# Kernel tuning notes

Hardware: AMD Instinct MI355X
Metric: run time of the kernel (lower is better)

The kernel has to match this reference:

```python
import jax, jax.numpy as jnp
import numpy as np

C = 512
HSIZE = C // 4
D, H, W = 18, 24, 24
N = D * H * W


def setup_inputs() -> dict:
    key = jax.random.key(0)
    ks = jax.random.split(key, 6)
    features = jax.random.normal(ks[0], (1, C, D, H, W), dtype=jnp.float32)
    Wi = jax.random.normal(ks[1], (HSIZE, C), dtype=jnp.float32) * 0.02
    bi = jax.random.normal(ks[2], (HSIZE,), dtype=jnp.float32) * 0.02
    Wj = jax.random.normal(ks[3], (HSIZE, C), dtype=jnp.float32) * 0.02
    bj = jax.random.normal(ks[4], (HSIZE,), dtype=jnp.float32) * 0.02
    # attention_agregate: shape (head=1, 1), xavier-uniform in the original
    agg = jax.random.uniform(ks[5], (1, 1), dtype=jnp.float32, minval=-1.0, maxval=1.0)
    return {"features": features, "Wi": Wi, "bi": bi, "Wj": Wj, "bj": bj, "agg": agg}


def reference(features, Wi, bi, Wj, bj, agg):
    # features: [1, C, D, H, W]; 1x1x1 convs == channel-wise matmuls
    x = features.reshape(C, N)                      # [C, N]
    fi = (Wi @ x + bi[:, None]).T                   # [N, hsize]  (conv_i output, permuted)
    fj = Wj @ x + bj[:, None]                       # [hsize, N]  (conv_j output)
    fk = x.T                                        # [N, C]      (raw features, NOT conv_k)
    # original: attn = (fi @ fj) * agg / N ; out = attn @ fk
    # linear chain reassociated: fi @ (fj @ fk) * agg / N  (same math, no NxN intermediate)
    scale = agg[0, 0] / jnp.float32(N)
    out_flat = (fi @ (fj @ fk)) * scale             # [N, C]
    return features + out_flat.T.reshape(1, C, D, H, W)
```

## Files before the change

### kernel.cpp

```cpp
#include <hip/hip_runtime.h>
#include <hip/hip_bf16.h>

#define C_   512
#define HS   128
#define NN   10368

typedef __bf16 bf16x8 __attribute__((ext_vector_type(8)));
typedef float  f32x4  __attribute__((ext_vector_type(4)));

__global__ void k_transpose(const float* __restrict__ x, __bf16* __restrict__ xbT,
                            float* __restrict__ Mtf) {
    const int b = blockIdx.x;
    const int t = threadIdx.x;
    if (b < 1296) {
        __shared__ float tile[64][65];
        const int c0 = (b & 7) * 64, n0 = (b >> 3) * 64;
        const int tr = t >> 6, tn = t & 63;
        #pragma unroll
        for (int i = 0; i < 16; i++) {
            int c = tr + i * 4;
            tile[c][tn] = x[(size_t)(c0 + c) * NN + n0 + tn];
        }
        __syncthreads();
        #pragma unroll
        for (int i = 0; i < 16; i++) {
            int n = tr + i * 4;
            xbT[(size_t)(n0 + n) * C_ + c0 + tn] = (__bf16)tile[tn][n];
        }
    } else {
        const int j = b - 1296;
        f32x4 z = {0.f, 0.f, 0.f, 0.f};
        float* p = Mtf + j * 4096 + t * 16;
        *(f32x4*)(p)      = z;
        *(f32x4*)(p + 4)  = z;
        *(f32x4*)(p + 8)  = z;
        *(f32x4*)(p + 12) = z;
    }
}

__device__ __forceinline__ bf16x8 load_f32x8_as_bf16(const float* __restrict__ p) {
    float4 v0 = *(const float4*)p;
    float4 v1 = *(const float4*)(p + 4);
    bf16x8 o;
    o[0] = (__bf16)v0.x; o[1] = (__bf16)v0.y; o[2] = (__bf16)v0.z; o[3] = (__bf16)v0.w;
    o[4] = (__bf16)v1.x; o[5] = (__bf16)v1.y; o[6] = (__bf16)v1.z; o[7] = (__bf16)v1.w;
    return o;
}

__global__ void k_gemm12(const __bf16* __restrict__ xbT,
                         const float* __restrict__ Wi, const float* __restrict__ Wj,
                         const float* __restrict__ bi, const float* __restrict__ bj,
                         __bf16* __restrict__ fj, __bf16* __restrict__ finm) {
    const int w    = blockIdx.x * 4 + (threadIdx.x >> 6);
    const int lane = threadIdx.x & 63;
    const int l16  = lane & 15;
    const int q    = lane >> 4;
    if (w < 648) {
        const int h0 = (w & 3) * 32, n0 = (w >> 2) * 64;
        f32x4 acc[2][4] = {};
        for (int k = 0; k < 512; k += 32) {
            bf16x8 a[2], b[4];
            #pragma unroll
            for (int i = 0; i < 2; i++)
                a[i] = load_f32x8_as_bf16(Wj + (h0 + 16 * i + l16) * 512 + k + q * 8);
            #pragma unroll
            for (int tt = 0; tt < 4; tt++)
                b[tt] = *(const bf16x8*)(xbT + (size_t)(n0 + 16 * tt + l16) * 512 + k + q * 8);
            #pragma unroll
            for (int i = 0; i < 2; i++)
                #pragma unroll
                for (int tt = 0; tt < 4; tt++)
                    acc[i][tt] = __builtin_amdgcn_mfma_f32_16x16x32_bf16(a[i], b[tt], acc[i][tt], 0, 0, 0);
        }
        #pragma unroll
        for (int i = 0; i < 2; i++)
            #pragma unroll
            for (int tt = 0; tt < 4; tt++)
                #pragma unroll
                for (int r = 0; r < 4; r++) {
                    int h = h0 + 16 * i + q * 4 + r;
                    int n = n0 + 16 * tt + l16;
                    fj[(size_t)h * NN + n] = (__bf16)(acc[i][tt][r] + bj[h]);
                }
    } else {
        const int w2 = w - 648;
        const int n0 = (w2 >> 2) * 64, h0 = (w2 & 3) * 32;
        f32x4 acc[4][2] = {};
        for (int k = 0; k < 512; k += 32) {
            bf16x8 a[4], b[2];
            #pragma unroll
            for (int i = 0; i < 4; i++)
                a[i] = *(const bf16x8*)(xbT + (size_t)(n0 + 16 * i + l16) * 512 + k + q * 8);
            #pragma unroll
            for (int tt = 0; tt < 2; tt++)
                b[tt] = load_f32x8_as_bf16(Wi + (h0 + 16 * tt + l16) * 512 + k + q * 8);
            #pragma unroll
            for (int i = 0; i < 4; i++)
                #pragma unroll
                for (int tt = 0; tt < 2; tt++)
                    acc[i][tt] = __builtin_amdgcn_mfma_f32_16x16x32_bf16(a[i], b[tt], acc[i][tt], 0, 0, 0);
        }
        #pragma unroll
        for (int i = 0; i < 4; i++)
            #pragma unroll
            for (int tt = 0; tt < 2; tt++)
                #pragma unroll
                for (int r = 0; r < 4; r++) {
                    int n = n0 + 16 * i + q * 4 + r;
                    int h = h0 + 16 * tt + l16;
                    finm[(size_t)n * HS + h] = (__bf16)(acc[i][tt][r] + bi[h]);
                }
    }
}

__global__ void k_gemm3(const float* __restrict__ feat, const __bf16* __restrict__ fj,
                        float* __restrict__ Mtf) {
    __shared__ float red[4][64][17];
    const int b    = blockIdx.x;
    const int t    = threadIdx.x;
    const int v    = t >> 6;
    const int lane = t & 63;
    const int l16  = lane & 15;
    const int q    = lane >> 4;
    const int tile = b & 63, g = b >> 6;
    const int c0 = (tile >> 2) * 32, h0 = (tile & 3) * 32;
    const int chunk = g * 4 + v;
    const int s0 = (chunk * 324) >> 5;
    const int s1 = ((chunk + 1) * 324) >> 5;
    f32x4 acc[2][2] = {};
    for (int s = s0; s < s1; s++) {
        int k = s * 32;
        bf16x8 a[2], bb[2];
        #pragma unroll
        for (int i = 0; i < 2; i++)
            a[i] = load_f32x8_as_bf16(feat + (size_t)(c0 + 16 * i + l16) * NN + k + q * 8);
        #pragma unroll
        for (int tt = 0; tt < 2; tt++)
            bb[tt] = *(const bf16x8*)(fj + (size_t)(h0 + 16 * tt + l16) * NN + k + q * 8);
        #pragma unroll
        for (int i = 0; i < 2; i++)
            #pragma unroll
            for (int tt = 0; tt < 2; tt++)
                acc[i][tt] = __builtin_amdgcn_mfma_f32_16x16x32_bf16(a[i], bb[tt], acc[i][tt], 0, 0, 0);
    }
    #pragma unroll
    for (int i = 0; i < 2; i++)
        #pragma unroll
        for (int tt = 0; tt < 2; tt++)
            #pragma unroll
            for (int r = 0; r < 4; r++)
                red[v][lane][i * 8 + tt * 4 + r] = acc[i][tt][r];
    __syncthreads();
    #pragma unroll
    for (int u = 0; u < 4; u++) {
        const int idx = t * 4 + u;
        const int lane_e = idx >> 4, j = idx & 15;
        float s = red[0][lane_e][j] + red[1][lane_e][j]
                + red[2][lane_e][j] + red[3][lane_e][j];
        const int i = j >> 3, tt = (j >> 2) & 1, r = j & 3;
        const int qe = lane_e >> 4, le = lane_e & 15;
        const int c = c0 + 16 * i + qe * 4 + r;
        const int h = h0 + 16 * tt + le;
        atomicAdd(&Mtf[c * HS + h], s);
    }
}

__global__ void k_gemm4(const float* __restrict__ Mtf, const __bf16* __restrict__ finm,
                        const float* __restrict__ feat, const float* __restrict__ agg,
                        float* __restrict__ out) {
    const int w    = blockIdx.x * 4 + (threadIdx.x >> 6);
    const int lane = threadIdx.x & 63;
    const int l16  = lane & 15;
    const int q    = lane >> 4;
    const int c0 = (w & 15) * 32, n0 = (w >> 4) * 64;
    const float scale = agg[0] * (1.0f / (float)NN);
    f32x4 acc[2][4] = {};
    for (int k = 0; k < 128; k += 32) {
        bf16x8 a[2], b[4];
        #pragma unroll
        for (int i = 0; i < 2; i++)
            a[i] = load_f32x8_as_bf16(Mtf + (c0 + 16 * i + l16) * HS + k + q * 8);
        #pragma unroll
        for (int tt = 0; tt < 4; tt++)
            b[tt] = *(const bf16x8*)(finm + (size_t)(n0 + 16 * tt + l16) * HS + k + q * 8);
        #pragma unroll
        for (int i = 0; i < 2; i++)
            #pragma unroll
            for (int tt = 0; tt < 4; tt++)
                acc[i][tt] = __builtin_amdgcn_mfma_f32_16x16x32_bf16(a[i], b[tt], acc[i][tt], 0, 0, 0);
    }
    #pragma unroll
    for (int i = 0; i < 2; i++)
        #pragma unroll
        for (int tt = 0; tt < 4; tt++)
            #pragma unroll
            for (int r = 0; r < 4; r++) {
                int c = c0 + 16 * i + q * 4 + r;
                int n = n0 + 16 * tt + l16;
                size_t idx = (size_t)c * NN + n;
                out[idx] = feat[idx] + scale * acc[i][tt][r];
            }
}

extern "C" void kernel_launch(void* const* d_in, const int* in_sizes, int n_in,
                              void* d_out, int out_size, void* d_ws, size_t ws_size,
                              hipStream_t stream) {
    const float* feat = (const float*)d_in[0];
    const float* Wi   = (const float*)d_in[1];
    const float* bi   = (const float*)d_in[2];
    const float* Wj   = (const float*)d_in[3];
    const float* bj   = (const float*)d_in[4];
    const float* agg  = (const float*)d_in[5];
    float* out = (float*)d_out;

    char* ws = (char*)d_ws;
    __bf16* xbT  = (__bf16*)(ws);
    __bf16* fj   = (__bf16*)(ws + 10616832);
    __bf16* finm = (__bf16*)(ws + 13271040);
    float*  Mtf  = (float*) (ws + 15925248);

    k_transpose<<<1312, 256, 0, stream>>>(feat, xbT, Mtf);
    k_gemm12<<<324, 256, 0, stream>>>(xbT, Wi, Wj, bi, bj, fj, finm);
    k_gemm3<<<512, 256, 0, stream>>>(feat, fj, Mtf);
    k_gemm4<<<648, 256, 0, stream>>>(Mtf, finm, feat, agg, out);
}
```

Before: 145.9 us.

## Fuse transpose into projection GEMMs via LDS staging and emit bf16 features for gemm3

```diff
diff --git a/kernel.cpp b/kernel.cpp
--- a/kernel.cpp
+++ b/kernel.cpp
@@ -6,37 +6,8 @@
 #define NN   10368
 
 typedef __bf16 bf16x8 __attribute__((ext_vector_type(8)));
+typedef __bf16 bf16x2 __attribute__((ext_vector_type(2)));
 typedef float  f32x4  __attribute__((ext_vector_type(4)));
-
-__global__ void k_transpose(const float* __restrict__ x, __bf16* __restrict__ xbT,
-                            float* __restrict__ Mtf) {
-    const int b = blockIdx.x;
-    const int t = threadIdx.x;
-    if (b < 1296) {
-        __shared__ float tile[64][65];
-        const int c0 = (b & 7) * 64, n0 = (b >> 3) * 64;
-        const int tr = t >> 6, tn = t & 63;
-        #pragma unroll
-        for (int i = 0; i < 16; i++) {
-            int c = tr + i * 4;
-            tile[c][tn] = x[(size_t)(c0 + c) * NN + n0 + tn];
-        }
-        __syncthreads();
-        #pragma unroll
-        for (int i = 0; i < 16; i++) {
-            int n = tr + i * 4;
-            xbT[(size_t)(n0 + n) * C_ + c0 + tn] = (__bf16)tile[tn][n];
-        }
-    } else {
-        const int j = b - 1296;
-        f32x4 z = {0.f, 0.f, 0.f, 0.f};
-        float* p = Mtf + j * 4096 + t * 16;
-        *(f32x4*)(p)      = z;
-        *(f32x4*)(p + 4)  = z;
-        *(f32x4*)(p + 8)  = z;
-        *(f32x4*)(p + 12) = z;
-    }
-}
 
 __device__ __forceinline__ bf16x8 load_f32x8_as_bf16(const float* __restrict__ p) {
     float4 v0 = *(const float4*)p;
@@ -47,73 +18,84 @@
     return o;
 }
 
-__global__ void k_gemm12(const __bf16* __restrict__ xbT,
-                         const float* __restrict__ Wi, const float* __restrict__ Wj,
-                         const float* __restrict__ bi, const float* __restrict__ bj,
-                         __bf16* __restrict__ fj, __bf16* __restrict__ finm) {
-    const int w    = blockIdx.x * 4 + (threadIdx.x >> 6);
-    const int lane = threadIdx.x & 63;
+__global__ void k_fused12(const float* __restrict__ feat,
+                          const float* __restrict__ Wi, const float* __restrict__ Wj,
+                          const float* __restrict__ bi, const float* __restrict__ bj,
+                          __bf16* __restrict__ xb, __bf16* __restrict__ fj,
+                          __bf16* __restrict__ finm, float* __restrict__ Mtf) {
+    const int b = blockIdx.x;
+    const int t = threadIdx.x;
+    if (b >= 324) {
+        const int j = b - 324;
+        f32x4 z = {0.f, 0.f, 0.f, 0.f};
+        float* p = Mtf + j * 4096 + t * 16;
+        *(f32x4*)(p) = z; *(f32x4*)(p + 4) = z;
+        *(f32x4*)(p + 8) = z; *(f32x4*)(p + 12) = z;
+        return;
+    }
+    __shared__ __bf16 xt[32][520];
+    const int n0 = b * 32;
+    {
+        const int tn = t & 31;
+        const int c2 = (t >> 5) * 2;
+        for (int cc = 0; cc < 512; cc += 16) {
+            const int c = cc + c2;
+            float v0 = feat[(size_t)c * NN + n0 + tn];
+            float v1 = feat[(size_t)(c + 1) * NN + n0 + tn];
+            __bf16 b0 = (__bf16)v0, b1 = (__bf16)v1;
+            xb[(size_t)c * NN + n0 + tn]       = b0;
+            xb[(size_t)(c + 1) * NN + n0 + tn] = b1;
+            bf16x2 pk; pk[0] = b0; pk[1] = b1;
+            *(bf16x2*)&xt[tn][c] = pk;
+        }
+    }
+    __syncthreads();
+    const int w    = t >> 6;
+    const int lane = t & 63;
     const int l16  = lane & 15;
     const int q    = lane >> 4;
-    if (w < 648) {
-        const int h0 = (w & 3) * 32, n0 = (w >> 2) * 64;
-        f32x4 acc[2][4] = {};
-        for (int k = 0; k < 512; k += 32) {
-            bf16x8 a[2], b[4];
-            #pragma unroll
-            for (int i = 0; i < 2; i++)
-                a[i] = load_f32x8_as_bf16(Wj + (h0 + 16 * i + l16) * 512 + k + q * 8);
-            #pragma unroll
-            for (int tt = 0; tt < 4; tt++)
-                b[tt] = *(const bf16x8*)(xbT + (size_t)(n0 + 16 * tt + l16) * 512 + k + q * 8);
-            #pragma unroll
-            for (int i = 0; i < 2; i++)
-                #pragma unroll
-                for (int tt = 0; tt < 4; tt++)
-                    acc[i][tt] = __builtin_amdgcn_mfma_f32_16x16x32_bf16(a[i], b[tt], acc[i][tt], 0, 0, 0);
-        }
-        #pragma unroll
-        for (int i = 0; i < 2; i++)
-            #pragma unroll
-            for (int tt = 0; tt < 4; tt++)
-                #pragma unroll
-                for (int r = 0; r < 4; r++) {
+    const int h0   = w * 32;
+    f32x4 afj[2][2] = {};
+    f32x4 afi[2][2] = {};
+    for (int k = 0; k < 512; k += 32) {
+        bf16x8 ln[2], wj[2], wi[2];
+        #pragma unroll
+        for (int i = 0; i < 2; i++)
+            ln[i] = *(const bf16x8*)&xt[16 * i + l16][k + q * 8];
+        #pragma unroll
+        for (int i = 0; i < 2; i++)
+            wj[i] = load_f32x8_as_bf16(Wj + (h0 + 16 * i + l16) * 512 + k + q * 8);
+        #pragma unroll
+        for (int i = 0; i < 2; i++)
+            wi[i] = load_f32x8_as_bf16(Wi + (h0 + 16 * i + l16) * 512 + k + q * 8);
+        #pragma unroll
+        for (int i = 0; i < 2; i++)
+            #pragma unroll
+            for (int tt = 0; tt < 2; tt++) {
+                afj[i][tt] = __builtin_amdgcn_mfma_f32_16x16x32_bf16(wj[i], ln[tt], afj[i][tt], 0, 0, 0);
+                afi[i][tt] = __builtin_amdgcn_mfma_f32_16x16x32_bf16(ln[i], wi[tt], afi[i][tt], 0, 0, 0);
+            }
+    }
+    #pragma unroll
+    for (int i = 0; i < 2; i++)
+        #pragma unroll
+        for (int tt = 0; tt < 2; tt++)
+            #pragma unroll
+            for (int r = 0; r < 4; r++) {
+                {
                     int h = h0 + 16 * i + q * 4 + r;
                     int n = n0 + 16 * tt + l16;
-                    fj[(size_t)h * NN + n] = (__bf16)(acc[i][tt][r] + bj[h]);
+                    fj[(size_t)h * NN + n] = (__bf16)(afj[i][tt][r] + bj[h]);
                 }
-    } else {
-        const int w2 = w - 648;
-        const int n0 = (w2 >> 2) * 64, h0 = (w2 & 3) * 32;
-        f32x4 acc[4][2] = {};
-        for (int k = 0; k < 512; k += 32) {
-            bf16x8 a[4], b[2];
-            #pragma unroll
-            for (int i = 0; i < 4; i++)
-                a[i] = *(const bf16x8*)(xbT + (size_t)(n0 + 16 * i + l16) * 512 + k + q * 8);
-            #pragma unroll
-            for (int tt = 0; tt < 2; tt++)
-                b[tt] = load_f32x8_as_bf16(Wi + (h0 + 16 * tt + l16) * 512 + k + q * 8);
-            #pragma unroll
-            for (int i = 0; i < 4; i++)
-                #pragma unroll
-                for (int tt = 0; tt < 2; tt++)
-                    acc[i][tt] = __builtin_amdgcn_mfma_f32_16x16x32_bf16(a[i], b[tt], acc[i][tt], 0, 0, 0);
-        }
-        #pragma unroll
-        for (int i = 0; i < 4; i++)
-            #pragma unroll
-            for (int tt = 0; tt < 2; tt++)
-                #pragma unroll
-                for (int r = 0; r < 4; r++) {
+                {
                     int n = n0 + 16 * i + q * 4 + r;
                     int h = h0 + 16 * tt + l16;
-                    finm[(size_t)n * HS + h] = (__bf16)(acc[i][tt][r] + bi[h]);
+                    finm[(size_t)n * HS + h] = (__bf16)(afi[i][tt][r] + bi[h]);
                 }
-    }
-}
-
-__global__ void k_gemm3(const float* __restrict__ feat, const __bf16* __restrict__ fj,
+            }
+}
+
+__global__ void k_gemm3(const __bf16* __restrict__ xb, const __bf16* __restrict__ fj,
                         float* __restrict__ Mtf) {
     __shared__ float red[4][64][17];
     const int b    = blockIdx.x;
@@ -133,7 +115,7 @@
         bf16x8 a[2], bb[2];
         #pragma unroll
         for (int i = 0; i < 2; i++)
-            a[i] = load_f32x8_as_bf16(feat + (size_t)(c0 + 16 * i + l16) * NN + k + q * 8);
+            a[i] = *(const bf16x8*)(xb + (size_t)(c0 + 16 * i + l16) * NN + k + q * 8);
         #pragma unroll
         for (int tt = 0; tt < 2; tt++)
             bb[tt] = *(const bf16x8*)(fj + (size_t)(h0 + 16 * tt + l16) * NN + k + q * 8);
@@ -214,13 +196,12 @@
     float* out = (float*)d_out;
 
     char* ws = (char*)d_ws;
-    __bf16* xbT  = (__bf16*)(ws);
+    __bf16* xb   = (__bf16*)(ws);
     __bf16* fj   = (__bf16*)(ws + 10616832);
     __bf16* finm = (__bf16*)(ws + 13271040);
     float*  Mtf  = (float*) (ws + 15925248);
 
-    k_transpose<<<1312, 256, 0, stream>>>(feat, xbT, Mtf);
-    k_gemm12<<<324, 256, 0, stream>>>(xbT, Wi, Wj, bi, bj, fj, finm);
-    k_gemm3<<<512, 256, 0, stream>>>(feat, fj, Mtf);
+    k_fused12<<<340, 256, 0, stream>>>(feat, Wi, Wj, bi, bj, xb, fj, finm, Mtf);
+    k_gemm3<<<512, 256, 0, stream>>>(xb, fj, Mtf);
     k_gemm4<<<648, 256, 0, stream>>>(Mtf, finm, feat, agg, out);
 }
```

Measured after the change: 139.1 us. 1.05x faster.
